# Performance work log

Measured on AMD Instinct MI355X. Metric: run time of the kernel, lower is better.

## Reference

```python
import jax, jax.numpy as jnp
import numpy as np

N_NODES = 100000   # n_entities + n_users
N_REL = 16
N_EDGES = 1600000
D = 64             # entity_dim == relation_dim
DIMS = [64, 32, 16, 16, 8]
NEG_SLOPE = 0.01   # nn.LeakyReLU default
EPS = 1e-12        # F.normalize default eps


def setup_inputs() -> dict:
    key = jax.random.key(0)
    ks = jax.random.split(key, 16)
    def lin(k, i, o):
        return jax.random.normal(k, (i, o), jnp.float32) / np.sqrt(i)
    inp = {
        'emb': jax.random.normal(ks[0], (N_NODES, D), jnp.float32) * 0.1,
        'rel_embed': jax.random.normal(ks[1], (N_REL, D), jnp.float32) * 0.1,
        'W_R': jax.random.normal(ks[2], (N_REL, D, D), jnp.float32) / np.sqrt(D),
        'W0': lin(ks[3], DIMS[0], DIMS[1]), 'b0': jnp.zeros((DIMS[1],), jnp.float32),
        'W1': lin(ks[4], DIMS[1], DIMS[2]), 'b1': jnp.zeros((DIMS[2],), jnp.float32),
        'W2': lin(ks[5], DIMS[2], DIMS[3]), 'b2': jnp.zeros((DIMS[3],), jnp.float32),
        'W3': lin(ks[6], DIMS[3], DIMS[4]), 'b3': jnp.zeros((DIMS[4],), jnp.float32),
        'src': jax.random.randint(ks[7], (N_EDGES,), 0, N_NODES, jnp.int32),
        'dst': jnp.sort(jax.random.randint(ks[8], (N_EDGES,), 0, N_NODES, jnp.int32)),
        'etype': jax.random.randint(ks[9], (N_EDGES,), 0, N_REL, jnp.int32),
    }
    return inp


def _lrelu(x):
    return jnp.where(x >= 0, x, NEG_SLOPE * x)


def _l2norm(x):
    n = jnp.sqrt(jnp.sum(x * x, axis=1, keepdims=True))
    return x / jnp.maximum(n, EPS)


def reference(emb, rel_embed, W_R, W0, b0, W1, b1, W2, b2, W3, b3, src, dst, etype):
    N = emb.shape[0]
    # --- compute_attention: TransR-style per-edge score (vectorized over relations) ---
    # all_mul[n, r, :] = emb[n] @ W_R[r]  (equivalent to the per-relation loop)
    all_mul = jnp.einsum('nd,rdk->nrk', emb, W_R)          # (N, R, D)
    r_mul_t = all_mul[src, etype]                          # edges.src transformed (E, D)
    r_mul_h = all_mul[dst, etype]                          # edges.dst transformed (E, D)
    att = jnp.sum(r_mul_t * jnp.tanh(r_mul_h + rel_embed[etype]), axis=-1)  # (E,)
    # --- edge softmax grouped by destination node ---
    m = jax.ops.segment_max(att, dst, num_segments=N)
    e = jnp.exp(att - m[dst])
    s = jax.ops.segment_sum(e, dst, num_segments=N)
    att = (e / s[dst])[:, None]                            # (E, 1)

    Ws = [(W0, b0), (W1, b1), (W2, b2), (W3, b3)]
    results = []
    for index in range(1, 5):
        ego = emb
        all_embed = [ego]
        for i, (W, b) in enumerate(Ws):
            if i < index:
                # u_mul_e('node','att') + sum over incoming edges
                N_h = jax.ops.segment_sum(att * ego[src], dst, num_segments=N)
                ego = _lrelu((ego + N_h) @ W + b)          # gcn aggregator, type 0
            else:
                ego = _lrelu(ego @ W + b)                  # type 1: linear only
            all_embed.append(_l2norm(ego))
        results.append(jnp.concatenate(all_embed, axis=1))  # (N, 136)
    return jnp.stack(results)                               # (4, N, 136)
```

## Files before the change

kernel.cpp:

```cpp
#include <hip/hip_runtime.h>
#include <hip/hip_bf16.h>
#include <math.h>

#define N_NODES 100000
#define N_RELS 16
#define N_EDGES 1600000
#define OUTW 136
#define NEG_SLOPE 0.01f
#define RES ((size_t)N_NODES * OUTW)

typedef __attribute__((ext_vector_type(8))) short short8;
typedef __attribute__((ext_vector_type(4))) float f32x4;

__device__ __forceinline__ float lrelu(float x) { return x >= 0.f ? x : NEG_SLOPE * x; }
__device__ __forceinline__ float fast_rcp(float x) { return __builtin_amdgcn_rcpf(x); }
__device__ __forceinline__ float fast_tanh(float x) {
    float e = __expf(2.f * x);
    return 1.f - 2.f * fast_rcp(e + 1.f);
}
__device__ __forceinline__ unsigned short f2bf(float f) {
    union { float f; unsigned u; } v; v.f = f;
    unsigned x = v.u + 0x7FFF + ((v.u >> 16) & 1);
    return (unsigned short)(x >> 16);
}

__global__ __launch_bounds__(256) void k_prep(const float* __restrict__ emb, unsigned short* __restrict__ embB,
                                              const float* __restrict__ WR, unsigned short* __restrict__ WT,
                                              const float* __restrict__ W0, const float* __restrict__ W1,
                                              const float* __restrict__ W2, const float* __restrict__ W3,
                                              float* __restrict__ WLT,
                                              const int* __restrict__ dst, int* __restrict__ offs,
                                              int* __restrict__ cnt) {
    int blk = blockIdx.x, tid = threadIdx.x;
    if (blk < 6250) {
        int id = blk * 256 + tid;
        float4 v = *(const float4*)(emb + (size_t)id * 4);
        ushort4 o; o.x = f2bf(v.x); o.y = f2bf(v.y); o.z = f2bf(v.z); o.w = f2bf(v.w);
        *(ushort4*)(embB + (size_t)id * 4) = o;
    } else if (blk < 6506) {
        int id = (blk - 6250) * 256 + tid;
        int r = id >> 12, rem = id & 4095, n = rem >> 6, k = rem & 63;
        WT[id] = f2bf(WR[(r << 12) + (k << 6) + n]);
    } else if (blk < 6518) {
        int id = (blk - 6506) * 256 + tid;
        if (id < 2944) {
            float v;
            if (id < 2048)      { int c = id >> 6, k = id & 63;                  v = W0[k * 32 + c]; }
            else if (id < 2560) { int r = id - 2048; int c = r >> 5, k = r & 31; v = W1[k * 16 + c]; }
            else if (id < 2816) { int r = id - 2560; int c = r >> 4, k = r & 15; v = W2[k * 16 + c]; }
            else                { int r = id - 2816; int c = r >> 4, k = r & 15; v = W3[k * 8 + c]; }
            WLT[id] = v;
        }
    } else if (blk < 6909) {
        int n = (blk - 6518) * 256 + tid;
        if (n <= N_NODES) {
            int lo = 0, hi = N_EDGES;
            while (lo < hi) { int mid = (lo + hi) >> 1; if (dst[mid] < n) lo = mid + 1; else hi = mid; }
            offs[n] = lo;
        }
    } else {
        if (tid < 16) cnt[tid] = 0;
    }
}

__global__ __launch_bounds__(256) void k_hist(const int* __restrict__ etype, int* __restrict__ cnt) {
    __shared__ int lcnt[16];
    int tid = threadIdx.x;
    if (tid < 16) lcnt[tid] = 0;
    __syncthreads();
    atomicAdd(&lcnt[etype[blockIdx.x * 256 + tid]], 1);
    __syncthreads();
    if (tid < 16 && lcnt[tid]) atomicAdd(&cnt[tid], lcnt[tid]);
}

__global__ void k_scan(const int* __restrict__ cnt, int* __restrict__ roff, int* __restrict__ cur) {
    if (threadIdx.x == 0) {
        int a = 0;
        for (int r = 0; r < 16; ++r) { roff[r] = a; cur[r] = a; a += cnt[r]; }
        roff[16] = a;
    }
}

__global__ __launch_bounds__(256) void k_scatter(const int* __restrict__ etype,
                                                 const int* __restrict__ src,
                                                 const int* __restrict__ dst,
                                                 int* __restrict__ cur, int* __restrict__ eperm,
                                                 int* __restrict__ srcp, int* __restrict__ dstp) {
    __shared__ int lcnt[16], lbase[16], loff[16];
    int tid = threadIdx.x;
    if (tid < 16) { lcnt[tid] = 0; loff[tid] = 0; }
    __syncthreads();
    int e = blockIdx.x * 256 + tid;
    int t = etype[e];
    atomicAdd(&lcnt[t], 1);
    __syncthreads();
    if (tid < 16) lbase[tid] = lcnt[tid] ? atomicAdd(&cur[tid], lcnt[tid]) : 0;
    __syncthreads();
    int rank = atomicAdd(&loff[t], 1);
    int pos = lbase[t] + rank;
    eperm[pos] = e;
    srcp[pos] = src[e];
    dstp[pos] = dst[e];
}

__global__ __launch_bounds__(256) void k_edge_attF(const unsigned short* __restrict__ embB,
                                                   const unsigned short* __restrict__ WT,
                                                   const float* __restrict__ rel,
                                                   const int* __restrict__ srcp,
                                                   const int* __restrict__ dstp,
                                                   const int* __restrict__ eperm,
                                                   const int* __restrict__ roff,
                                                   float* __restrict__ att) {
    int tid = threadIdx.x, w = tid >> 6, l = tid & 63;
    int rlo = l & 15, rhi = l >> 4;
    int r = blockIdx.x >> 7;
    int blk = blockIdx.x & 127;
    int lo = roff[r], hi = roff[r + 1];
    int nb = (hi - lo + 15) >> 4;
    constexpr int STEP = 512;

    const unsigned short* wt = WT + ((size_t)r << 12);
    short8 bfr[4][2];
    float relv[4];
    #pragma unroll
    for (int cb = 0; cb < 4; ++cb) {
        bfr[cb][0] = *(const short8*)(wt + (cb * 16 + rlo) * 64 + rhi * 8);
        bfr[cb][1] = *(const short8*)(wt + (cb * 16 + rlo) * 64 + 32 + rhi * 8);
        relv[cb] = rel[r * 64 + cb * 16 + rlo];
    }

    int g0 = blk * 4 + w;
    if (g0 >= nb) return;

    auto ldidx = [&](int g, int& sa, int& sb) {
        int ea = lo + g * 16 + rlo;
        if (ea >= hi) ea = hi - 1;
        sa = srcp[ea]; sb = dstp[ea];
    };

    int saC, sbC, saN, sbN;
    ldidx(g0, saC, sbC);
    if (g0 + STEP < nb) ldidx(g0 + STEP, saN, sbN); else { saN = saC; sbN = sbC; }

    short8 at0 = *(const short8*)(embB + (size_t)saC * 64 + rhi * 8);
    short8 at1 = *(const short8*)(embB + (size_t)saC * 64 + 32 + rhi * 8);
    short8 ah0 = *(const short8*)(embB + (size_t)sbC * 64 + rhi * 8);
    short8 ah1 = *(const short8*)(embB + (size_t)sbC * 64 + 32 + rhi * 8);

    for (int g = g0; g < nb; g += STEP) {
        short8 nt0, nt1, nh0, nh1;
        bool hasn = (g + STEP) < nb;
        if (hasn) {
            nt0 = *(const short8*)(embB + (size_t)saN * 64 + rhi * 8);
            nt1 = *(const short8*)(embB + (size_t)saN * 64 + 32 + rhi * 8);
            nh0 = *(const short8*)(embB + (size_t)sbN * 64 + rhi * 8);
            nh1 = *(const short8*)(embB + (size_t)sbN * 64 + 32 + rhi * 8);
        }
        if (g + 2 * STEP < nb) ldidx(g + 2 * STEP, saN, sbN);

        f32x4 accT[4], accH[4];
        #pragma unroll
        for (int cb = 0; cb < 4; ++cb) {
            accT[cb] = (f32x4){0.f, 0.f, 0.f, 0.f};
            accH[cb] = (f32x4){0.f, 0.f, 0.f, 0.f};
            accT[cb] = __builtin_amdgcn_mfma_f32_16x16x32_bf16(at0, bfr[cb][0], accT[cb], 0, 0, 0);
            accT[cb] = __builtin_amdgcn_mfma_f32_16x16x32_bf16(at1, bfr[cb][1], accT[cb], 0, 0, 0);
            accH[cb] = __builtin_amdgcn_mfma_f32_16x16x32_bf16(ah0, bfr[cb][0], accH[cb], 0, 0, 0);
            accH[cb] = __builtin_amdgcn_mfma_f32_16x16x32_bf16(ah1, bfr[cb][1], accH[cb], 0, 0, 0);
        }
        int i0 = lo + g * 16;
        #pragma unroll
        for (int i = 0; i < 4; ++i) {
            float s = 0.f;
            #pragma unroll
            for (int cb = 0; cb < 4; ++cb)
                s += accT[cb][i] * fast_tanh(accH[cb][i] + relv[cb]);
            s += __shfl_xor(s, 1); s += __shfl_xor(s, 2);
            s += __shfl_xor(s, 4); s += __shfl_xor(s, 8);
            int idx = i0 + rhi * 4 + i;
            if (rlo == 0 && idx < hi) att[eperm[idx]] = s;
        }
        at0 = nt0; at1 = nt1; ah0 = nh0; ah1 = nh1;
    }
}

__global__ __launch_bounds__(256) void k_softmax(float* __restrict__ att, const int* __restrict__ offs) {
    int tid = threadIdx.x;
    int n = blockIdx.x * 32 + (tid >> 3);
    int j = tid & 7;
    int b = offs[n], e = offs[n + 1];
    if (b >= e) return;
    float m = -INFINITY;
    for (int i = b + j; i < e; i += 8) m = fmaxf(m, att[i]);
    #pragma unroll
    for (int s = 4; s >= 1; s >>= 1) m = fmaxf(m, __shfl_xor(m, s));
    float sum = 0.f;
    for (int i = b + j; i < e; i += 8) { float v = __expf(att[i] - m); att[i] = v; sum += v; }
    #pragma unroll
    for (int s = 4; s >= 1; s >>= 1) sum += __shfl_xor(sum, s);
    float inv = fast_rcp(sum);
    for (int i = b + j; i < e; i += 8) att[i] *= inv;
}

__global__ __launch_bounds__(256) void k_dense0(const float* __restrict__ emb,
                                                const float* __restrict__ WLT,
                                                float* __restrict__ Y0,
                                                float* __restrict__ out) {
    int tid = threadIdx.x, w = tid >> 6, l = tid & 63;
    int c = l & 31, g = l >> 5;
    float Wreg[32];
    #pragma unroll
    for (int kk = 0; kk < 32; ++kk) Wreg[kk] = WLT[(size_t)c * 64 + g * 32 + kk];
    int nw = gridDim.x * 4;
    for (int n = blockIdx.x * 4 + w; n < N_NODES; n += nw) {
        const float* xr = emb + (size_t)n * 64;
        float v = xr[l];
        #pragma unroll
        for (int r = 0; r < 4; ++r)
            out[(size_t)r * RES + (size_t)n * OUTW + l] = v;
        float o = 0.f;
        #pragma unroll
        for (int kk = 0; kk < 32; kk += 4) {
            float4 xv = *(const float4*)(xr + g * 32 + kk);
            o += xv.x * Wreg[kk] + xv.y * Wreg[kk + 1] + xv.z * Wreg[kk + 2] + xv.w * Wreg[kk + 3];
        }
        o += __shfl_xor(o, 32);
        if (l < 32) Y0[(size_t)n * 32 + c] = o;
    }
}

template<int D, int DN, int COL, int RSTART, bool PROJ>
__global__ __launch_bounds__(256) void k_aggF(const float* __restrict__ Y,
                                              const float* __restrict__ att,
                                              const int* __restrict__ src,
                                              const int* __restrict__ offs,
                                              const float* __restrict__ bias,
                                              const float* __restrict__ WTn,
                                              float* __restrict__ Yn,
                                              float* __restrict__ out) {
    constexpr int E = D / 4;
    constexpr int S = 64 / E;
    constexpr int G = PROJ ? (64 / DN) : 1;
    constexpr int KS = PROJ ? (D / G) : 1;
    __shared__ float xm[4][PROJ ? D : 4];
    int tid = threadIdx.x, w = tid >> 6, l = tid & 63;
    int n = blockIdx.x * 4 + w;
    int b = offs[n], e = offs[n + 1];
    int je = l & (E - 1), slot = l / E;

    float Wreg[KS];
    if constexpr (PROJ) {
        int c = l & (DN - 1), g = l / DN;
        #pragma unroll
        for (int kk = 0; kk < KS; ++kk) Wreg[kk] = WTn[(size_t)c * D + g * KS + kk];
    }

    float4 a = make_float4(0.f, 0.f, 0.f, 0.f);
    int i = b + slot;
    for (; i + S < e; i += 2 * S) {
        float t0 = att[i], t1 = att[i + S];
        float4 p0 = *(const float4*)(Y + (size_t)src[i]     * D + 4 * je);
        float4 p1 = *(const float4*)(Y + (size_t)src[i + S] * D + 4 * je);
        a.x += t0 * p0.x + t1 * p1.x;
        a.y += t0 * p0.y + t1 * p1.y;
        a.z += t0 * p0.z + t1 * p1.z;
        a.w += t0 * p0.w + t1 * p1.w;
    }
    for (; i < e; i += S) {
        float t0 = att[i];
        float4 p0 = *(const float4*)(Y + (size_t)src[i] * D + 4 * je);
        a.x += t0 * p0.x; a.y += t0 * p0.y; a.z += t0 * p0.z; a.w += t0 * p0.w;
    }
    #pragma unroll
    for (int st = E; st < 64; st <<= 1) {
        a.x += __shfl_xor(a.x, st); a.y += __shfl_xor(a.y, st);
        a.z += __shfl_xor(a.z, st); a.w += __shfl_xor(a.w, st);
    }
    float4 q  = *(const float4*)(Y + (size_t)n * D + 4 * je);
    float4 bi = *(const float4*)(bias + 4 * je);
    float4 u;
    u.x = lrelu(a.x + q.x + bi.x);
    u.y = lrelu(a.y + q.y + bi.y);
    u.z = lrelu(a.z + q.z + bi.z);
    u.w = lrelu(a.w + q.w + bi.w);
    float ss = u.x * u.x + u.y * u.y + u.z * u.z + u.w * u.w;
    #pragma unroll
    for (int st = 1; st < E; st <<= 1) ss += __shfl_xor(ss, st);
    float inv = fast_rcp(fmaxf(sqrtf(ss), 1e-12f));
    if (slot < 4 - RSTART) {
        float4 nr = make_float4(u.x * inv, u.y * inv, u.z * inv, u.w * inv);
        *(float4*)(out + (size_t)(RSTART + slot) * RES + (size_t)n * OUTW + COL + 4 * je) = nr;
    }
    if constexpr (PROJ) {
        if (slot == S - 1) *(float4*)&xm[w][4 * je] = u;
        __builtin_amdgcn_s_waitcnt(0);
        __builtin_amdgcn_sched_barrier(0);
        int c = l & (DN - 1), g = l / DN;
        float o = 0.f;
        if constexpr (KS >= 4) {
            #pragma unroll
            for (int kk = 0; kk < KS; kk += 4) {
                float4 xv = *(const float4*)&xm[w][g * KS + kk];
                o += xv.x * Wreg[kk] + xv.y * Wreg[kk + 1] + xv.z * Wreg[kk + 2] + xv.w * Wreg[kk + 3];
            }
        } else {
            float2 xv = *(const float2*)&xm[w][g * KS];
            o += xv.x * Wreg[0] + xv.y * Wreg[1];
        }
        #pragma unroll
        for (int st = DN; st < 64; st <<= 1) o += __shfl_xor(o, st);
        if (l < DN) Yn[(size_t)n * DN + c] = o;
    }
}

__global__ __launch_bounds__(256) void k_bchain(const float* __restrict__ Y1,
                                                const float* __restrict__ Y2,
                                                const float* __restrict__ Y3,
                                                const float* __restrict__ WLT,
                                                const float* __restrict__ b1,
                                                const float* __restrict__ b2,
                                                const float* __restrict__ b3,
                                                float* __restrict__ out) {
    __shared__ float W2s[16][17], W3s[8][17];
    __shared__ float bb1[16], bb2[16], bb3[8];
    __shared__ float mid[16][17], mid2[16][17];
    int tid = threadIdx.x;
    if (tid < 256) W2s[tid >> 4][tid & 15] = WLT[2560 + tid];
    if (tid < 128) W3s[tid >> 4][tid & 15] = WLT[2816 + tid];
    if (tid < 16) bb1[tid] = b1[tid];
    if (tid >= 32 && tid < 48) bb2[tid - 32] = b2[tid - 32];
    if (tid >= 64 && tid < 72) bb3[tid - 64] = b3[tid - 64];
    __syncthreads();

    int grp = tid >> 4, lj = tid & 15;
    int seg = blockIdx.x / 6250;
    int nb = blockIdx.x % 6250;
    int n = nb * 16 + grp;

    if (seg == 0) {
        float u1 = lrelu(Y1[(size_t)n * 16 + lj] + bb1[lj]);
        mid[grp][lj] = u1;
        float ss = u1 * u1;
        #pragma unroll
        for (int m = 8; m >= 1; m >>= 1) ss += __shfl_xor(ss, m);
        out[(size_t)n * OUTW + 96 + lj] = u1 * fast_rcp(fmaxf(sqrtf(ss), 1e-12f));
        __builtin_amdgcn_s_waitcnt(0);
        __builtin_amdgcn_sched_barrier(0);
        float o2 = bb2[lj];
        #pragma unroll
        for (int k = 0; k < 16; ++k) o2 += mid[grp][k] * W2s[lj][k];
        float u2 = lrelu(o2);
        mid2[grp][lj] = u2;
        float s2 = u2 * u2;
        #pragma unroll
        for (int m = 8; m >= 1; m >>= 1) s2 += __shfl_xor(s2, m);
        out[(size_t)n * OUTW + 112 + lj] = u2 * fast_rcp(fmaxf(sqrtf(s2), 1e-12f));
        __builtin_amdgcn_s_waitcnt(0);
        __builtin_amdgcn_sched_barrier(0);
        if (lj < 8) {
            float o3 = bb3[lj];
            #pragma unroll
            for (int k = 0; k < 16; ++k) o3 += mid2[grp][k] * W3s[lj][k];
            float u3 = lrelu(o3);
            float s3 = u3 * u3;
            #pragma unroll
            for (int m = 4; m >= 1; m >>= 1) s3 += __shfl_xor(s3, m);
            out[(size_t)n * OUTW + 128 + lj] = u3 * fast_rcp(fmaxf(sqrtf(s3), 1e-12f));
        }
    } else if (seg == 1) {
        float u2 = lrelu(Y2[(size_t)n * 16 + lj] + bb2[lj]);
        mid[grp][lj] = u2;
        float s2 = u2 * u2;
        #pragma unroll
        for (int m = 8; m >= 1; m >>= 1) s2 += __shfl_xor(s2, m);
        out[RES + (size_t)n * OUTW + 112 + lj] = u2 * fast_rcp(fmaxf(sqrtf(s2), 1e-12f));
        __builtin_amdgcn_s_waitcnt(0);
        __builtin_amdgcn_sched_barrier(0);
        if (lj < 8) {
            float o3 = bb3[lj];
            #pragma unroll
            for (int k = 0; k < 16; ++k) o3 += mid[grp][k] * W3s[lj][k];
            float u3 = lrelu(o3);
            float s3 = u3 * u3;
            #pragma unroll
            for (int m = 4; m >= 1; m >>= 1) s3 += __shfl_xor(s3, m);
            out[RES + (size_t)n * OUTW + 128 + lj] = u3 * fast_rcp(fmaxf(sqrtf(s3), 1e-12f));
        }
    } else {
        if (lj < 8) {
            float u3 = lrelu(Y3[(size_t)n * 8 + lj] + bb3[lj]);
            float s3 = u3 * u3;
            #pragma unroll
            for (int m = 4; m >= 1; m >>= 1) s3 += __shfl_xor(s3, m);
            out[2 * RES + (size_t)n * OUTW + 128 + lj] = u3 * fast_rcp(fmaxf(sqrtf(s3), 1e-12f));
        }
    }
}

extern "C" void kernel_launch(void* const* d_in, const int* in_sizes, int n_in,
                              void* d_out, int out_size, void* d_ws, size_t ws_size,
                              hipStream_t stream) {
    (void)in_sizes; (void)n_in; (void)out_size; (void)ws_size;
    const float* emb = (const float*)d_in[0];
    const float* rel_embed = (const float*)d_in[1];
    const float* W_R = (const float*)d_in[2];
    const float* W0 = (const float*)d_in[3];  const float* b0 = (const float*)d_in[4];
    const float* W1 = (const float*)d_in[5];  const float* b1 = (const float*)d_in[6];
    const float* W2 = (const float*)d_in[7];  const float* b2 = (const float*)d_in[8];
    const float* W3 = (const float*)d_in[9];  const float* b3 = (const float*)d_in[10];
    const int* src = (const int*)d_in[11];
    const int* dst = (const int*)d_in[12];
    const int* etype = (const int*)d_in[13];
    float* out = (float*)d_out;

    char* p = (char*)d_ws;
    auto alloc = [&](size_t bytes) { char* q = p; p += (bytes + 255) & ~(size_t)255; return q; };
    int* offs  = (int*)alloc((size_t)(N_NODES + 1) * 4);
    float* att = (float*)alloc((size_t)N_EDGES * 4);
    int* eperm = (int*)alloc((size_t)N_EDGES * 4);
    int* srcp  = (int*)alloc((size_t)N_EDGES * 4);
    int* dstp  = (int*)alloc((size_t)N_EDGES * 4);
    int* cnt   = (int*)alloc(64);
    int* roff  = (int*)alloc(68);
    int* cur   = (int*)alloc(64);
    unsigned short* embB = (unsigned short*)alloc((size_t)N_NODES * 64 * 2);
    unsigned short* WT   = (unsigned short*)alloc((size_t)65536 * 2);
    float* WLT = (float*)alloc((size_t)2944 * 4);
    float* Y0  = (float*)alloc((size_t)N_NODES * 32 * 4);
    float* Y1  = (float*)alloc((size_t)N_NODES * 16 * 4);
    float* Y2  = (float*)alloc((size_t)N_NODES * 16 * 4);
    float* Y3  = (float*)alloc((size_t)N_NODES * 8 * 4);

    k_prep<<<6910, 256, 0, stream>>>(emb, embB, W_R, WT, W0, W1, W2, W3, WLT, dst, offs, cnt);
    k_hist<<<N_EDGES / 256, 256, 0, stream>>>(etype, cnt);
    k_scan<<<1, 64, 0, stream>>>(cnt, roff, cur);
    k_scatter<<<N_EDGES / 256, 256, 0, stream>>>(etype, src, dst, cur, eperm, srcp, dstp);

    k_edge_attF<<<16 * 128, 256, 0, stream>>>(embB, WT, rel_embed, srcp, dstp, eperm, roff, att);
    k_softmax<<<N_NODES / 32, 256, 0, stream>>>(att, offs);

    k_dense0<<<3125, 256, 0, stream>>>(emb, WLT, Y0, out);

    k_aggF<32, 16,  64, 0, true ><<<N_NODES / 4, 256, 0, stream>>>(Y0, att, src, offs, b0, WLT + 2048, Y1, out);
    k_aggF<16, 16,  96, 1, true ><<<N_NODES / 4, 256, 0, stream>>>(Y1, att, src, offs, b1, WLT + 2560, Y2, out);
    k_aggF<16,  8, 112, 2, true ><<<N_NODES / 4, 256, 0, stream>>>(Y2, att, src, offs, b2, WLT + 2816, Y3, out);
    k_aggF< 8,  8, 128, 3, false><<<N_NODES / 4, 256, 0, stream>>>(Y3, att, src, offs, b3, nullptr, nullptr, out);

    k_bchain<<<18750, 256, 0, stream>>>(Y1, Y2, Y3, WLT, b1, b2, b3, out);
}
```

Measured before the change: 527.6 us.

## Fuse launches: merge hist into prep, softmax into first aggregation, dense0 with attention

```diff
diff --git a/kernel.cpp b/kernel.cpp
--- a/kernel.cpp
+++ b/kernel.cpp
@@ -30,7 +30,7 @@
                                               const float* __restrict__ W2, const float* __restrict__ W3,
                                               float* __restrict__ WLT,
                                               const int* __restrict__ dst, int* __restrict__ offs,
-                                              int* __restrict__ cnt) {
+                                              const int* __restrict__ etype, int* __restrict__ cnt) {
     int blk = blockIdx.x, tid = threadIdx.x;
     if (blk < 6250) {
         int id = blk * 256 + tid;
@@ -59,18 +59,13 @@
             offs[n] = lo;
         }
     } else {
-        if (tid < 16) cnt[tid] = 0;
-    }
-}
-
-__global__ __launch_bounds__(256) void k_hist(const int* __restrict__ etype, int* __restrict__ cnt) {
-    __shared__ int lcnt[16];
-    int tid = threadIdx.x;
-    if (tid < 16) lcnt[tid] = 0;
-    __syncthreads();
-    atomicAdd(&lcnt[etype[blockIdx.x * 256 + tid]], 1);
-    __syncthreads();
-    if (tid < 16 && lcnt[tid]) atomicAdd(&cnt[tid], lcnt[tid]);
+        __shared__ int lcnt[16];
+        if (tid < 16) lcnt[tid] = 0;
+        __syncthreads();
+        atomicAdd(&lcnt[etype[(blk - 6909) * 256 + tid]], 1);
+        __syncthreads();
+        if (tid < 16 && lcnt[tid]) atomicAdd(&cnt[tid], lcnt[tid]);
+    }
 }
 
 __global__ void k_scan(const int* __restrict__ cnt, int* __restrict__ roff, int* __restrict__ cur) {
@@ -103,130 +98,195 @@
     dstp[pos] = dst[e];
 }
 
-__global__ __launch_bounds__(256) void k_edge_attF(const unsigned short* __restrict__ embB,
+__global__ __launch_bounds__(256) void k_att_dense(const unsigned short* __restrict__ embB,
                                                    const unsigned short* __restrict__ WT,
                                                    const float* __restrict__ rel,
                                                    const int* __restrict__ srcp,
                                                    const int* __restrict__ dstp,
                                                    const int* __restrict__ eperm,
                                                    const int* __restrict__ roff,
-                                                   float* __restrict__ att) {
+                                                   float* __restrict__ att,
+                                                   const float* __restrict__ emb,
+                                                   const float* __restrict__ WLT,
+                                                   float* __restrict__ Y0,
+                                                   float* __restrict__ out) {
     int tid = threadIdx.x, w = tid >> 6, l = tid & 63;
-    int rlo = l & 15, rhi = l >> 4;
-    int r = blockIdx.x >> 7;
-    int blk = blockIdx.x & 127;
-    int lo = roff[r], hi = roff[r + 1];
-    int nb = (hi - lo + 15) >> 4;
-    constexpr int STEP = 512;
-
-    const unsigned short* wt = WT + ((size_t)r << 12);
-    short8 bfr[4][2];
-    float relv[4];
-    #pragma unroll
-    for (int cb = 0; cb < 4; ++cb) {
-        bfr[cb][0] = *(const short8*)(wt + (cb * 16 + rlo) * 64 + rhi * 8);
-        bfr[cb][1] = *(const short8*)(wt + (cb * 16 + rlo) * 64 + 32 + rhi * 8);
-        relv[cb] = rel[r * 64 + cb * 16 + rlo];
-    }
-
-    int g0 = blk * 4 + w;
-    if (g0 >= nb) return;
-
-    auto ldidx = [&](int g, int& sa, int& sb) {
-        int ea = lo + g * 16 + rlo;
-        if (ea >= hi) ea = hi - 1;
-        sa = srcp[ea]; sb = dstp[ea];
-    };
-
-    int saC, sbC, saN, sbN;
-    ldidx(g0, saC, sbC);
-    if (g0 + STEP < nb) ldidx(g0 + STEP, saN, sbN); else { saN = saC; sbN = sbC; }
-
-    short8 at0 = *(const short8*)(embB + (size_t)saC * 64 + rhi * 8);
-    short8 at1 = *(const short8*)(embB + (size_t)saC * 64 + 32 + rhi * 8);
-    short8 ah0 = *(const short8*)(embB + (size_t)sbC * 64 + rhi * 8);
-    short8 ah1 = *(const short8*)(embB + (size_t)sbC * 64 + 32 + rhi * 8);
-
-    for (int g = g0; g < nb; g += STEP) {
-        short8 nt0, nt1, nh0, nh1;
-        bool hasn = (g + STEP) < nb;
-        if (hasn) {
-            nt0 = *(const short8*)(embB + (size_t)saN * 64 + rhi * 8);
-            nt1 = *(const short8*)(embB + (size_t)saN * 64 + 32 + rhi * 8);
-            nh0 = *(const short8*)(embB + (size_t)sbN * 64 + rhi * 8);
-            nh1 = *(const short8*)(embB + (size_t)sbN * 64 + 32 + rhi * 8);
-        }
-        if (g + 2 * STEP < nb) ldidx(g + 2 * STEP, saN, sbN);
-
-        f32x4 accT[4], accH[4];
+    if (blockIdx.x < 2048) {
+        int rlo = l & 15, rhi = l >> 4;
+        int r = blockIdx.x >> 7;
+        int blk = blockIdx.x & 127;
+        int lo = roff[r], hi = roff[r + 1];
+        int nb = (hi - lo + 15) >> 4;
+        constexpr int STEP = 512;
+
+        const unsigned short* wt = WT + ((size_t)r << 12);
+        short8 bfr[4][2];
+        float relv[4];
         #pragma unroll
         for (int cb = 0; cb < 4; ++cb) {
-            accT[cb] = (f32x4){0.f, 0.f, 0.f, 0.f};
-            accH[cb] = (f32x4){0.f, 0.f, 0.f, 0.f};
-            accT[cb] = __builtin_amdgcn_mfma_f32_16x16x32_bf16(at0, bfr[cb][0], accT[cb], 0, 0, 0);
-            accT[cb] = __builtin_amdgcn_mfma_f32_16x16x32_bf16(at1, bfr[cb][1], accT[cb], 0, 0, 0);
-            accH[cb] = __builtin_amdgcn_mfma_f32_16x16x32_bf16(ah0, bfr[cb][0], accH[cb], 0, 0, 0);
-            accH[cb] = __builtin_amdgcn_mfma_f32_16x16x32_bf16(ah1, bfr[cb][1], accH[cb], 0, 0, 0);
-        }
-        int i0 = lo + g * 16;
+            bfr[cb][0] = *(const short8*)(wt + (cb * 16 + rlo) * 64 + rhi * 8);
+            bfr[cb][1] = *(const short8*)(wt + (cb * 16 + rlo) * 64 + 32 + rhi * 8);
+            relv[cb] = rel[r * 64 + cb * 16 + rlo];
+        }
+
+        int g0 = blk * 4 + w;
+        if (g0 >= nb) return;
+
+        auto ldidx = [&](int g, int& sa, int& sb) {
+            int ea = lo + g * 16 + rlo;
+            if (ea >= hi) ea = hi - 1;
+            sa = srcp[ea]; sb = dstp[ea];
+        };
+
+        int saC, sbC, saN, sbN;
+        ldidx(g0, saC, sbC);
+        if (g0 + STEP < nb) ldidx(g0 + STEP, saN, sbN); else { saN = saC; sbN = sbC; }
+
+        short8 at0 = *(const short8*)(embB + (size_t)saC * 64 + rhi * 8);
+        short8 at1 = *(const short8*)(embB + (size_t)saC * 64 + 32 + rhi * 8);
+        short8 ah0 = *(const short8*)(embB + (size_t)sbC * 64 + rhi * 8);
+        short8 ah1 = *(const short8*)(embB + (size_t)sbC * 64 + 32 + rhi * 8);
+
+        for (int g = g0; g < nb; g += STEP) {
+            short8 nt0, nt1, nh0, nh1;
+            bool hasn = (g + STEP) < nb;
+            if (hasn) {
+                nt0 = *(const short8*)(embB + (size_t)saN * 64 + rhi * 8);
+                nt1 = *(const short8*)(embB + (size_t)saN * 64 + 32 + rhi * 8);
+                nh0 = *(const short8*)(embB + (size_t)sbN * 64 + rhi * 8);
+                nh1 = *(const short8*)(embB + (size_t)sbN * 64 + 32 + rhi * 8);
+            }
+            if (g + 2 * STEP < nb) ldidx(g + 2 * STEP, saN, sbN);
+
+            f32x4 accT[4], accH[4];
+            #pragma unroll
+            for (int cb = 0; cb < 4; ++cb) {
+                accT[cb] = (f32x4){0.f, 0.f, 0.f, 0.f};
+                accH[cb] = (f32x4){0.f, 0.f, 0.f, 0.f};
+                accT[cb] = __builtin_amdgcn_mfma_f32_16x16x32_bf16(at0, bfr[cb][0], accT[cb], 0, 0, 0);
+                accT[cb] = __builtin_amdgcn_mfma_f32_16x16x32_bf16(at1, bfr[cb][1], accT[cb], 0, 0, 0);
+                accH[cb] = __builtin_amdgcn_mfma_f32_16x16x32_bf16(ah0, bfr[cb][0], accH[cb], 0, 0, 0);
+                accH[cb] = __builtin_amdgcn_mfma_f32_16x16x32_bf16(ah1, bfr[cb][1], accH[cb], 0, 0, 0);
+            }
+            int i0 = lo + g * 16;
+            #pragma unroll
+            for (int i = 0; i < 4; ++i) {
+                float s = 0.f;
+                #pragma unroll
+                for (int cb = 0; cb < 4; ++cb)
+                    s += accT[cb][i] * fast_tanh(accH[cb][i] + relv[cb]);
+                s += __shfl_xor(s, 1); s += __shfl_xor(s, 2);
+                s += __shfl_xor(s, 4); s += __shfl_xor(s, 8);
+                int idx = i0 + rhi * 4 + i;
+                if (rlo == 0 && idx < hi) att[eperm[idx]] = s;
+            }
+            at0 = nt0; at1 = nt1; ah0 = nh0; ah1 = nh1;
+        }
+    } else {
+        int bid = blockIdx.x - 2048;
+        int c = l & 31, g = l >> 5;
+        float Wreg[32];
         #pragma unroll
-        for (int i = 0; i < 4; ++i) {
-            float s = 0.f;
-            #pragma unroll
-            for (int cb = 0; cb < 4; ++cb)
-                s += accT[cb][i] * fast_tanh(accH[cb][i] + relv[cb]);
-            s += __shfl_xor(s, 1); s += __shfl_xor(s, 2);
-            s += __shfl_xor(s, 4); s += __shfl_xor(s, 8);
-            int idx = i0 + rhi * 4 + i;
-            if (rlo == 0 && idx < hi) att[eperm[idx]] = s;
-        }
-        at0 = nt0; at1 = nt1; ah0 = nh0; ah1 = nh1;
-    }
-}
-
-__global__ __launch_bounds__(256) void k_softmax(float* __restrict__ att, const int* __restrict__ offs) {
-    int tid = threadIdx.x;
-    int n = blockIdx.x * 32 + (tid >> 3);
-    int j = tid & 7;
+        for (int kk = 0; kk < 32; ++kk) Wreg[kk] = WLT[(size_t)c * 64 + g * 32 + kk];
+        for (int n = bid * 4 + w; n < N_NODES; n += 12500) {
+            const float* xr = emb + (size_t)n * 64;
+            float v = xr[l];
+            #pragma unroll
+            for (int r = 0; r < 4; ++r)
+                out[(size_t)r * RES + (size_t)n * OUTW + l] = v;
+            float o = 0.f;
+            #pragma unroll
+            for (int kk = 0; kk < 32; kk += 4) {
+                float4 xv = *(const float4*)(xr + g * 32 + kk);
+                o += xv.x * Wreg[kk] + xv.y * Wreg[kk + 1] + xv.z * Wreg[kk + 2] + xv.w * Wreg[kk + 3];
+            }
+            o += __shfl_xor(o, 32);
+            if (l < 32) Y0[(size_t)n * 32 + c] = o;
+        }
+    }
+}
+
+__global__ __launch_bounds__(256) void k_aggF1(const float* __restrict__ Y,
+                                               const float* __restrict__ att,
+                                               float* __restrict__ attn,
+                                               const int* __restrict__ src,
+                                               const int* __restrict__ offs,
+                                               const float* __restrict__ bias,
+                                               const float* __restrict__ WTn,
+                                               float* __restrict__ Yn,
+                                               float* __restrict__ out) {
+    constexpr int D = 32, DN = 16, E = 8, S = 8, KS = 8;
+    __shared__ float xm[4][D];
+    int tid = threadIdx.x, w = tid >> 6, l = tid & 63;
+    int n = blockIdx.x * 4 + w;
     int b = offs[n], e = offs[n + 1];
-    if (b >= e) return;
+    int je = l & (E - 1), slot = l / E;
+    int c = l & (DN - 1), g = l / DN;
+
+    float Wreg[KS];
+    #pragma unroll
+    for (int kk = 0; kk < KS; ++kk) Wreg[kk] = WTn[(size_t)c * D + g * KS + kk];
+
     float m = -INFINITY;
-    for (int i = b + j; i < e; i += 8) m = fmaxf(m, att[i]);
-    #pragma unroll
-    for (int s = 4; s >= 1; s >>= 1) m = fmaxf(m, __shfl_xor(m, s));
+    for (int i = b + l; i < e; i += 64) m = fmaxf(m, att[i]);
+    #pragma unroll
+    for (int st = 32; st >= 1; st >>= 1) m = fmaxf(m, __shfl_xor(m, st));
     float sum = 0.f;
-    for (int i = b + j; i < e; i += 8) { float v = __expf(att[i] - m); att[i] = v; sum += v; }
-    #pragma unroll
-    for (int s = 4; s >= 1; s >>= 1) sum += __shfl_xor(sum, s);
+    for (int i = b + l; i < e; i += 64) sum += __expf(att[i] - m);
+    #pragma unroll
+    for (int st = 32; st >= 1; st >>= 1) sum += __shfl_xor(sum, st);
     float inv = fast_rcp(sum);
-    for (int i = b + j; i < e; i += 8) att[i] *= inv;
-}
-
-__global__ __launch_bounds__(256) void k_dense0(const float* __restrict__ emb,
-                                                const float* __restrict__ WLT,
-                                                float* __restrict__ Y0,
-                                                float* __restrict__ out) {
-    int tid = threadIdx.x, w = tid >> 6, l = tid & 63;
-    int c = l & 31, g = l >> 5;
-    float Wreg[32];
-    #pragma unroll
-    for (int kk = 0; kk < 32; ++kk) Wreg[kk] = WLT[(size_t)c * 64 + g * 32 + kk];
-    int nw = gridDim.x * 4;
-    for (int n = blockIdx.x * 4 + w; n < N_NODES; n += nw) {
-        const float* xr = emb + (size_t)n * 64;
-        float v = xr[l];
-        #pragma unroll
-        for (int r = 0; r < 4; ++r)
-            out[(size_t)r * RES + (size_t)n * OUTW + l] = v;
-        float o = 0.f;
-        #pragma unroll
-        for (int kk = 0; kk < 32; kk += 4) {
-            float4 xv = *(const float4*)(xr + g * 32 + kk);
-            o += xv.x * Wreg[kk] + xv.y * Wreg[kk + 1] + xv.z * Wreg[kk + 2] + xv.w * Wreg[kk + 3];
-        }
-        o += __shfl_xor(o, 32);
-        if (l < 32) Y0[(size_t)n * 32 + c] = o;
-    }
+
+    float4 a = make_float4(0.f, 0.f, 0.f, 0.f);
+    int i = b + slot;
+    for (; i + S < e; i += 2 * S) {
+        float t0 = __expf(att[i] - m) * inv, t1 = __expf(att[i + S] - m) * inv;
+        if (je == 0) { attn[i] = t0; attn[i + S] = t1; }
+        float4 p0 = *(const float4*)(Y + (size_t)src[i]     * D + 4 * je);
+        float4 p1 = *(const float4*)(Y + (size_t)src[i + S] * D + 4 * je);
+        a.x += t0 * p0.x + t1 * p1.x;
+        a.y += t0 * p0.y + t1 * p1.y;
+        a.z += t0 * p0.z + t1 * p1.z;
+        a.w += t0 * p0.w + t1 * p1.w;
+    }
+    for (; i < e; i += S) {
+        float t0 = __expf(att[i] - m) * inv;
+        if (je == 0) attn[i] = t0;
+        float4 p0 = *(const float4*)(Y + (size_t)src[i] * D + 4 * je);
+        a.x += t0 * p0.x; a.y += t0 * p0.y; a.z += t0 * p0.z; a.w += t0 * p0.w;
+    }
+    #pragma unroll
+    for (int st = E; st < 64; st <<= 1) {
+        a.x += __shfl_xor(a.x, st); a.y += __shfl_xor(a.y, st);
+        a.z += __shfl_xor(a.z, st); a.w += __shfl_xor(a.w, st);
+    }
+    float4 q  = *(const float4*)(Y + (size_t)n * D + 4 * je);
+    float4 bi = *(const float4*)(bias + 4 * je);
+    float4 u;
+    u.x = lrelu(a.x + q.x + bi.x);
+    u.y = lrelu(a.y + q.y + bi.y);
+    u.z = lrelu(a.z + q.z + bi.z);
+    u.w = lrelu(a.w + q.w + bi.w);
+    float ss = u.x * u.x + u.y * u.y + u.z * u.z + u.w * u.w;
+    #pragma unroll
+    for (int st = 1; st < E; st <<= 1) ss += __shfl_xor(ss, st);
+    float nv = fast_rcp(fmaxf(sqrtf(ss), 1e-12f));
+    if (slot < 4) {
+        float4 nr = make_float4(u.x * nv, u.y * nv, u.z * nv, u.w * nv);
+        *(float4*)(out + (size_t)slot * RES + (size_t)n * OUTW + 64 + 4 * je) = nr;
+    }
+    if (slot == S - 1) *(float4*)&xm[w][4 * je] = u;
+    __builtin_amdgcn_s_waitcnt(0);
+    __builtin_amdgcn_sched_barrier(0);
+    float o = 0.f;
+    #pragma unroll
+    for (int kk = 0; kk < KS; kk += 4) {
+        float4 xv = *(const float4*)&xm[w][g * KS + kk];
+        o += xv.x * Wreg[kk] + xv.y * Wreg[kk + 1] + xv.z * Wreg[kk + 2] + xv.w * Wreg[kk + 3];
+    }
+    #pragma unroll
+    for (int st = DN; st < 64; st <<= 1) o += __shfl_xor(o, st);
+    if (l < DN) Yn[(size_t)n * DN + c] = o;
 }
 
 template<int D, int DN, int COL, int RSTART, bool PROJ>
@@ -313,86 +373,133 @@
     }
 }
 
-__global__ __launch_bounds__(256) void k_bchain(const float* __restrict__ Y1,
-                                                const float* __restrict__ Y2,
-                                                const float* __restrict__ Y3,
-                                                const float* __restrict__ WLT,
-                                                const float* __restrict__ b1,
-                                                const float* __restrict__ b2,
-                                                const float* __restrict__ b3,
-                                                float* __restrict__ out) {
-    __shared__ float W2s[16][17], W3s[8][17];
-    __shared__ float bb1[16], bb2[16], bb3[8];
-    __shared__ float mid[16][17], mid2[16][17];
+__global__ __launch_bounds__(256) void k_tail(const float* __restrict__ Y3,
+                                              const float* __restrict__ attn,
+                                              const int* __restrict__ src,
+                                              const int* __restrict__ offs,
+                                              const float* __restrict__ b3v,
+                                              const float* __restrict__ Y1,
+                                              const float* __restrict__ Y2,
+                                              const float* __restrict__ WLT,
+                                              const float* __restrict__ b1,
+                                              const float* __restrict__ b2,
+                                              float* __restrict__ out) {
     int tid = threadIdx.x;
-    if (tid < 256) W2s[tid >> 4][tid & 15] = WLT[2560 + tid];
-    if (tid < 128) W3s[tid >> 4][tid & 15] = WLT[2816 + tid];
-    if (tid < 16) bb1[tid] = b1[tid];
-    if (tid >= 32 && tid < 48) bb2[tid - 32] = b2[tid - 32];
-    if (tid >= 64 && tid < 72) bb3[tid - 64] = b3[tid - 64];
-    __syncthreads();
-
-    int grp = tid >> 4, lj = tid & 15;
-    int seg = blockIdx.x / 6250;
-    int nb = blockIdx.x % 6250;
-    int n = nb * 16 + grp;
-
-    if (seg == 0) {
-        float u1 = lrelu(Y1[(size_t)n * 16 + lj] + bb1[lj]);
-        mid[grp][lj] = u1;
-        float ss = u1 * u1;
+    if (blockIdx.x < 25000) {
+        constexpr int D = 8, E = 2, S = 32;
+        int w = tid >> 6, l = tid & 63;
+        int n = blockIdx.x * 4 + w;
+        int b = offs[n], e = offs[n + 1];
+        int je = l & (E - 1), slot = l / E;
+        float4 a = make_float4(0.f, 0.f, 0.f, 0.f);
+        int i = b + slot;
+        for (; i + S < e; i += 2 * S) {
+            float t0 = attn[i], t1 = attn[i + S];
+            float4 p0 = *(const float4*)(Y3 + (size_t)src[i]     * D + 4 * je);
+            float4 p1 = *(const float4*)(Y3 + (size_t)src[i + S] * D + 4 * je);
+            a.x += t0 * p0.x + t1 * p1.x;
+            a.y += t0 * p0.y + t1 * p1.y;
+            a.z += t0 * p0.z + t1 * p1.z;
+            a.w += t0 * p0.w + t1 * p1.w;
+        }
+        for (; i < e; i += S) {
+            float t0 = attn[i];
+            float4 p0 = *(const float4*)(Y3 + (size_t)src[i] * D + 4 * je);
+            a.x += t0 * p0.x; a.y += t0 * p0.y; a.z += t0 * p0.z; a.w += t0 * p0.w;
+        }
         #pragma unroll
-        for (int m = 8; m >= 1; m >>= 1) ss += __shfl_xor(ss, m);
-        out[(size_t)n * OUTW + 96 + lj] = u1 * fast_rcp(fmaxf(sqrtf(ss), 1e-12f));
-        __builtin_amdgcn_s_waitcnt(0);
-        __builtin_amdgcn_sched_barrier(0);
-        float o2 = bb2[lj];
-        #pragma unroll
-        for (int k = 0; k < 16; ++k) o2 += mid[grp][k] * W2s[lj][k];
-        float u2 = lrelu(o2);
-        mid2[grp][lj] = u2;
-        float s2 = u2 * u2;
-        #pragma unroll
-        for (int m = 8; m >= 1; m >>= 1) s2 += __shfl_xor(s2, m);
-        out[(size_t)n * OUTW + 112 + lj] = u2 * fast_rcp(fmaxf(sqrtf(s2), 1e-12f));
-        __builtin_amdgcn_s_waitcnt(0);
-        __builtin_amdgcn_sched_barrier(0);
-        if (lj < 8) {
-            float o3 = bb3[lj];
-            #pragma unroll
-            for (int k = 0; k < 16; ++k) o3 += mid2[grp][k] * W3s[lj][k];
-            float u3 = lrelu(o3);
-            float s3 = u3 * u3;
-            #pragma unroll
-            for (int m = 4; m >= 1; m >>= 1) s3 += __shfl_xor(s3, m);
-            out[(size_t)n * OUTW + 128 + lj] = u3 * fast_rcp(fmaxf(sqrtf(s3), 1e-12f));
-        }
-    } else if (seg == 1) {
-        float u2 = lrelu(Y2[(size_t)n * 16 + lj] + bb2[lj]);
-        mid[grp][lj] = u2;
-        float s2 = u2 * u2;
-        #pragma unroll
-        for (int m = 8; m >= 1; m >>= 1) s2 += __shfl_xor(s2, m);
-        out[RES + (size_t)n * OUTW + 112 + lj] = u2 * fast_rcp(fmaxf(sqrtf(s2), 1e-12f));
-        __builtin_amdgcn_s_waitcnt(0);
-        __builtin_amdgcn_sched_barrier(0);
-        if (lj < 8) {
-            float o3 = bb3[lj];
-            #pragma unroll
-            for (int k = 0; k < 16; ++k) o3 += mid[grp][k] * W3s[lj][k];
-            float u3 = lrelu(o3);
-            float s3 = u3 * u3;
-            #pragma unroll
-            for (int m = 4; m >= 1; m >>= 1) s3 += __shfl_xor(s3, m);
-            out[RES + (size_t)n * OUTW + 128 + lj] = u3 * fast_rcp(fmaxf(sqrtf(s3), 1e-12f));
+        for (int st = E; st < 64; st <<= 1) {
+            a.x += __shfl_xor(a.x, st); a.y += __shfl_xor(a.y, st);
+            a.z += __shfl_xor(a.z, st); a.w += __shfl_xor(a.w, st);
+        }
+        float4 q  = *(const float4*)(Y3 + (size_t)n * D + 4 * je);
+        float4 bi = *(const float4*)(b3v + 4 * je);
+        float4 u;
+        u.x = lrelu(a.x + q.x + bi.x);
+        u.y = lrelu(a.y + q.y + bi.y);
+        u.z = lrelu(a.z + q.z + bi.z);
+        u.w = lrelu(a.w + q.w + bi.w);
+        float ss = u.x * u.x + u.y * u.y + u.z * u.z + u.w * u.w;
+        ss += __shfl_xor(ss, 1);
+        float inv = fast_rcp(fmaxf(sqrtf(ss), 1e-12f));
+        if (slot < 1) {
+            float4 nr = make_float4(u.x * inv, u.y * inv, u.z * inv, u.w * inv);
+            *(float4*)(out + 3 * RES + (size_t)n * OUTW + 128 + 4 * je) = nr;
         }
     } else {
-        if (lj < 8) {
-            float u3 = lrelu(Y3[(size_t)n * 8 + lj] + bb3[lj]);
-            float s3 = u3 * u3;
-            #pragma unroll
-            for (int m = 4; m >= 1; m >>= 1) s3 += __shfl_xor(s3, m);
-            out[2 * RES + (size_t)n * OUTW + 128 + lj] = u3 * fast_rcp(fmaxf(sqrtf(s3), 1e-12f));
+        __shared__ float W2s[16][17], W3s[8][17];
+        __shared__ float bb1[16], bb2[16], bb3[8];
+        __shared__ float mid[16][17], mid2[16][17];
+        if (tid < 256) W2s[tid >> 4][tid & 15] = WLT[2560 + tid];
+        if (tid < 128) W3s[tid >> 4][tid & 15] = WLT[2816 + tid];
+        if (tid < 16) bb1[tid] = b1[tid];
+        if (tid >= 32 && tid < 48) bb2[tid - 32] = b2[tid - 32];
+        if (tid >= 64 && tid < 72) bb3[tid - 64] = b3v[tid - 64];
+        __syncthreads();
+
+        int grp = tid >> 4, lj = tid & 15;
+        int bid = blockIdx.x - 25000;
+        int seg = bid / 6250;
+        int nb = bid % 6250;
+        int n = nb * 16 + grp;
+
+        if (seg == 0) {
+            float u1 = lrelu(Y1[(size_t)n * 16 + lj] + bb1[lj]);
+            mid[grp][lj] = u1;
+            float ss = u1 * u1;
+            #pragma unroll
+            for (int m = 8; m >= 1; m >>= 1) ss += __shfl_xor(ss, m);
+            out[(size_t)n * OUTW + 96 + lj] = u1 * fast_rcp(fmaxf(sqrtf(ss), 1e-12f));
+            __builtin_amdgcn_s_waitcnt(0);
+            __builtin_amdgcn_sched_barrier(0);
+            float o2 = bb2[lj];
+            #pragma unroll
+            for (int k = 0; k < 16; ++k) o2 += mid[grp][k] * W2s[lj][k];
+            float u2 = lrelu(o2);
+            mid2[grp][lj] = u2;
+            float s2 = u2 * u2;
+            #pragma unroll
+            for (int m = 8; m >= 1; m >>= 1) s2 += __shfl_xor(s2, m);
+            out[(size_t)n * OUTW + 112 + lj] = u2 * fast_rcp(fmaxf(sqrtf(s2), 1e-12f));
+            __builtin_amdgcn_s_waitcnt(0);
+            __builtin_amdgcn_sched_barrier(0);
+            if (lj < 8) {
+                float o3 = bb3[lj];
+                #pragma unroll
+                for (int k = 0; k < 16; ++k) o3 += mid2[grp][k] * W3s[lj][k];
+                float u3 = lrelu(o3);
+                float s3 = u3 * u3;
+                #pragma unroll
+                for (int m = 4; m >= 1; m >>= 1) s3 += __shfl_xor(s3, m);
+                out[(size_t)n * OUTW + 128 + lj] = u3 * fast_rcp(fmaxf(sqrtf(s3), 1e-12f));
+            }
+        } else if (seg == 1) {
+            float u2 = lrelu(Y2[(size_t)n * 16 + lj] + bb2[lj]);
+            mid[grp][lj] = u2;
+            float s2 = u2 * u2;
+            #pragma unroll
+            for (int m = 8; m >= 1; m >>= 1) s2 += __shfl_xor(s2, m);
+            out[RES + (size_t)n * OUTW + 112 + lj] = u2 * fast_rcp(fmaxf(sqrtf(s2), 1e-12f));
+            __builtin_amdgcn_s_waitcnt(0);
+            __builtin_amdgcn_sched_barrier(0);
+            if (lj < 8) {
+                float o3 = bb3[lj];
+                #pragma unroll
+                for (int k = 0; k < 16; ++k) o3 += mid[grp][k] * W3s[lj][k];
+                float u3 = lrelu(o3);
+                float s3 = u3 * u3;
+                #pragma unroll
+                for (int m = 4; m >= 1; m >>= 1) s3 += __shfl_xor(s3, m);
+                out[RES + (size_t)n * OUTW + 128 + lj] = u3 * fast_rcp(fmaxf(sqrtf(s3), 1e-12f));
+            }
+        } else {
+            if (lj < 8) {
+                float u3 = lrelu(Y3[(size_t)n * 8 + lj] + bb3[lj]);
+                float s3 = u3 * u3;
+                #pragma unroll
+                for (int m = 4; m >= 1; m >>= 1) s3 += __shfl_xor(s3, m);
+                out[2 * RES + (size_t)n * OUTW + 128 + lj] = u3 * fast_rcp(fmaxf(sqrtf(s3), 1e-12f));
+            }
         }
     }
 }
@@ -417,6 +524,7 @@
     auto alloc = [&](size_t bytes) { char* q = p; p += (bytes + 255) & ~(size_t)255; return q; };
     int* offs  = (int*)alloc((size_t)(N_NODES + 1) * 4);
     float* att = (float*)alloc((size_t)N_EDGES * 4);
+    float* attn = (float*)alloc((size_t)N_EDGES * 4);
     int* eperm = (int*)alloc((size_t)N_EDGES * 4);
     int* srcp  = (int*)alloc((size_t)N_EDGES * 4);
     int* dstp  = (int*)alloc((size_t)N_EDGES * 4);
@@ -431,20 +539,17 @@
     float* Y2  = (float*)alloc((size_t)N_NODES * 16 * 4);
     float* Y3  = (float*)alloc((size_t)N_NODES * 8 * 4);
 
-    k_prep<<<6910, 256, 0, stream>>>(emb, embB, W_R, WT, W0, W1, W2, W3, WLT, dst, offs, cnt);
-    k_hist<<<N_EDGES / 256, 256, 0, stream>>>(etype, cnt);
+    hipMemsetAsync(cnt, 0, 64, stream);
+    k_prep<<<13159, 256, 0, stream>>>(emb, embB, W_R, WT, W0, W1, W2, W3, WLT, dst, offs, etype, cnt);
     k_scan<<<1, 64, 0, stream>>>(cnt, roff, cur);
     k_scatter<<<N_EDGES / 256, 256, 0, stream>>>(etype, src, dst, cur, eperm, srcp, dstp);
 
-    k_edge_attF<<<16 * 128, 256, 0, stream>>>(embB, WT, rel_embed, srcp, dstp, eperm, roff, att);
-    k_softmax<<<N_NODES / 32, 256, 0, stream>>>(att, offs);
-
-    k_dense0<<<3125, 256, 0, stream>>>(emb, WLT, Y0, out);
-
-    k_aggF<32, 16,  64, 0, true ><<<N_NODES / 4, 256, 0, stream>>>(Y0, att, src, offs, b0, WLT + 2048, Y1, out);
-    k_aggF<16, 16,  96, 1, true ><<<N_NODES / 4, 256, 0, stream>>>(Y1, att, src, offs, b1, WLT + 2560, Y2, out);
-    k_aggF<16,  8, 112, 2, true ><<<N_NODES / 4, 256, 0, stream>>>(Y2, att, src, offs, b2, WLT + 2816, Y3, out);
-    k_aggF< 8,  8, 128, 3, false><<<N_NODES / 4, 256, 0, stream>>>(Y3, att, src, offs, b3, nullptr, nullptr, out);
-
-    k_bchain<<<18750, 256, 0, stream>>>(Y1, Y2, Y3, WLT, b1, b2, b3, out);
-}
+    k_att_dense<<<2048 + 3125, 256, 0, stream>>>(embB, WT, rel_embed, srcp, dstp, eperm, roff, att,
+                                                 emb, WLT, Y0, out);
+
+    k_aggF1<<<N_NODES / 4, 256, 0, stream>>>(Y0, att, attn, src, offs, b0, WLT + 2048, Y1, out);
+    k_aggF<16, 16,  96, 1, true ><<<N_NODES / 4, 256, 0, stream>>>(Y1, attn, src, offs, b1, WLT + 2560, Y2, out);
+    k_aggF<16,  8, 112, 2, true ><<<N_NODES / 4, 256, 0, stream>>>(Y2, attn, src, offs, b2, WLT + 2816, Y3, out);
+
+    k_tail<<<25000 + 18750, 256, 0, stream>>>(Y3, attn, src, offs, b3, Y1, Y2, WLT, b1, b2, out);
+}
```

Measured after the change: 518.8 us. Within noise of the previous version (-1.7%).
